# Kernel tuning notes

Measured on AMD Instinct MI355X. Metric: run time of the kernel, lower is better.

The kernel has to match this reference:

```python
import jax, jax.numpy as jnp
import numpy as np

B, C_IN, C_MID, C_OUT, L = 32, 8, 128, 128, 512
T, DT = 50, 0.5
K = T // 2 + 1  # 26
DN = ('NCH', 'OIH', 'NCH')

def conv1d_same(x, w, b):
    # zero-padded 'SAME' Conv1d, kernel size 3
    y = jax.lax.conv_general_dilated(x, w, (1,), 'SAME', dimension_numbers=DN)
    return y + b[None, :, None]

def setup_inputs() -> dict:
    key = jax.random.key(0)
    ks = jax.random.split(key, 32)
    def n(k, shape, s=0.1):
        return jax.random.normal(k, shape, dtype=jnp.float32) * s
    inp = {}
    inp['x'] = jax.random.normal(ks[0], (B, C_IN, L), dtype=jnp.float32)
    # omega encoder (3 convs + ReLU)
    inp['ow1'] = n(ks[1], (C_MID, C_IN, 3));  inp['ob1'] = jnp.zeros((C_MID,), jnp.float32)
    inp['ow2'] = n(ks[2], (C_MID, C_MID, 3)); inp['ob2'] = jnp.zeros((C_MID,), jnp.float32)
    inp['ow3'] = n(ks[3], (C_OUT, C_MID, 3)); inp['ob3'] = jnp.zeros((C_OUT,), jnp.float32)
    # alpha encoder
    inp['aw1'] = n(ks[4], (C_MID, C_IN, 3));  inp['ab1'] = jnp.zeros((C_MID,), jnp.float32)
    inp['aw2'] = n(ks[5], (C_MID, C_MID, 3)); inp['ab2'] = jnp.zeros((C_MID,), jnp.float32)
    inp['aw3'] = n(ks[6], (C_OUT, C_MID, 3)); inp['ab3'] = jnp.zeros((C_OUT,), jnp.float32)
    # hy encoder (4 convs, last Tanh)
    inp['hw1'] = n(ks[7], (C_MID, C_IN, 3));  inp['hb1'] = jnp.zeros((C_MID,), jnp.float32)
    inp['hw2'] = n(ks[8], (C_MID, C_MID, 3)); inp['hb2'] = jnp.zeros((C_MID,), jnp.float32)
    inp['hw3'] = n(ks[9], (C_MID, C_MID, 3)); inp['hb3'] = jnp.zeros((C_MID,), jnp.float32)
    inp['hw4'] = n(ks[10], (C_OUT, C_MID, 3)); inp['hb4'] = jnp.zeros((C_OUT,), jnp.float32)
    # cell circular conv weight (no bias)
    inp['wy'] = n(ks[11], (C_OUT, C_OUT, 3))
    # linear readout
    inp['fct'] = n(ks[12], (K, T))                     # fc_time: T -> K, no bias
    inp['rw1'] = n(ks[13], (64, K * C_OUT)); inp['rb1'] = jnp.zeros((64,), jnp.float32)
    inp['rw2'] = n(ks[14], (32, 64));        inp['rb2'] = jnp.zeros((32,), jnp.float32)
    inp['rw3'] = n(ks[15], (1, 32));         inp['rb3'] = jnp.zeros((1,), jnp.float32)
    return inp

def reference(x, ow1, ob1, ow2, ob2, ow3, ob3,
              aw1, ab1, aw2, ab2, aw3, ab3,
              hw1, hb1, hw2, hb2, hw3, hb3, hw4, hb4,
              wy, fct, rw1, rb1, rw2, rb2, rw3, rb3):
    relu = jax.nn.relu
    omega = relu(conv1d_same(relu(conv1d_same(relu(conv1d_same(x, ow1, ob1)), ow2, ob2)), ow3, ob3))
    alpha = relu(conv1d_same(relu(conv1d_same(relu(conv1d_same(x, aw1, ab1)), aw2, ab2)), aw3, ab3))
    h = relu(conv1d_same(x, hw1, hb1))
    h = relu(conv1d_same(h, hw2, hb2))
    h = relu(conv1d_same(h, hw3, hb3))
    hy0 = jnp.tanh(conv1d_same(h, hw4, hb4))          # (B, C_OUT, L)
    hz0 = jnp.zeros_like(hy0)

    def circ_conv(h):
        # circular padding of 1 on each side, then VALID conv (matches padding_mode='circular')
        hp = jnp.concatenate([h[..., -1:], h, h[..., :1]], axis=-1)
        return jax.lax.conv_general_dilated(hp, wy, (1,), 'VALID', dimension_numbers=DN)

    def step(carry, _):
        hy, hz = carry
        spring = jnp.tanh(circ_conv(hy))
        hz = hz + DT * (spring - omega * hy - alpha * hz)
        hy = hy + DT * hz
        return (hy, hz), hy

    (_, _), ys = jax.lax.scan(step, (hy0, hz0), None, length=T)
    y_seq = jnp.transpose(ys, (1, 0, 2, 3))           # (B, T, C_OUT, L)

    # linear readout: fc_time over T, mean over L, MLP
    fft = jnp.einsum('btcl,kt->bkcl', y_seq, fct)     # (B, K, C_OUT, L)
    feat = fft.reshape(B, K * C_OUT, L).mean(axis=2)  # (B, K*C_OUT)
    h1 = relu(feat @ rw1.T + rb1)
    h2 = relu(h1 @ rw2.T + rb2)
    logits = h2 @ rw3.T + rb3                         # (B, 1)
    return logits, y_seq
```

## Files before the change

kernel.cpp:

```cpp
#include <hip/hip_runtime.h>
#include <math.h>

#define YB (50*128*512)
#define YT (128*512)
#define DTc 0.5f

typedef __attribute__((ext_vector_type(8))) short bf16x8;
typedef __attribute__((ext_vector_type(4))) float f32x4;

__device__ __forceinline__ unsigned short f2bf(float f) {
    unsigned int u = __builtin_bit_cast(unsigned int, f);
    u += 0x7fffu + ((u >> 16) & 1u);
    return (unsigned short)(u >> 16);
}
__device__ __forceinline__ float bf2f(unsigned short h) {
    unsigned int u = ((unsigned int)h) << 16;
    return __builtin_bit_cast(float, u);
}

__device__ __forceinline__ float tanh_fast(float x) {
    float ax = fabsf(x);
    float e  = __expf(-2.f * ax);
    float r  = (1.f - e) * __builtin_amdgcn_rcpf(1.f + e);
    return __builtin_copysignf(r, x);
}

__device__ __forceinline__ void lds_sync() {
    asm volatile("s_waitcnt lgkmcnt(0)" ::: "memory");
    __builtin_amdgcn_sched_barrier(0);
    __builtin_amdgcn_s_barrier();
    __builtin_amdgcn_sched_barrier(0);
}

struct WSrc { const float* p[11]; };
__global__ void wprep_all_k(WSrc s, float* __restrict__ wt) {
    int idx = blockIdx.x * 256 + threadIdx.x;
    if (idx < 9216) {
        int wsel = idx / 3072, r = idx % 3072;
        int row = r >> 7, co = r & 127;
        int ci = row / 3, k = row - ci * 3;
        wt[idx] = s.p[wsel][(co * 8 + ci) * 3 + k];
    } else if (idx < 9216 + 589824) {
        int q = idx - 9216;
        int cv = q / 49152, r = q % 49152;
        int co = r / 384, kap = r % 384;
        int k = kap >> 7;
        int ci = ((kap >> 5) & 3) * 32 + (kap & 31);
        const int selmap[12] = {10, 7, 8, 9, 3, 3, 4, 4, 5, 5, 6, 6};
        float w = s.p[selmap[cv]][(co * 128 + ci) * 3 + k];
        unsigned short hv = f2bf(w);
        unsigned short ov = ((cv >= 4) && (cv & 1)) ? f2bf(w - bf2f(hv)) : hv;
        ((unsigned short*)(wt + 9216))[q] = ov;
    }
}

struct Job { const float* src; float* dst; const float* wt; const float* bias; int sbs, dbs, act; };
struct Jobs3 { Job j[3]; };

__global__ __launch_bounds__(256) void conv8x3_k(Jobs3 js) {
    int jb = blockIdx.y % 3;
    Job jo = js.j[jb];
    int b = blockIdx.z, tile = blockIdx.x, tid = threadIdx.x;
    int l0 = tile * 64;
    int tl4 = (tid & 15) * 4;
    int co0 = (tid >> 4) * 8;
    __shared__ float xs[8 * 68];
    __shared__ float wsh[24 * 128];
    const float* sb = jo.src + (size_t)b * jo.sbs;
    for (int idx = tid; idx < 8 * 66; idx += 256) {
        int ci = idx / 66, ll = idx - ci * 66;
        int gl = l0 - 1 + ll;
        xs[ci * 68 + ll] = (gl >= 0 && gl < 512) ? sb[ci * 512 + gl] : 0.f;
    }
    for (int idx = tid; idx < 24 * 128; idx += 256) wsh[idx] = jo.wt[idx];
    __syncthreads();
    float acc[8][4] = {};
    #pragma unroll
    for (int ci = 0; ci < 8; ++ci) {
        float x6[6];
        #pragma unroll
        for (int j = 0; j < 6; ++j) x6[j] = xs[ci * 68 + tl4 + j];
        #pragma unroll
        for (int k = 0; k < 3; ++k) {
            float w8[8];
            #pragma unroll
            for (int i = 0; i < 8; ++i) w8[i] = wsh[(ci * 3 + k) * 128 + co0 + i];
            #pragma unroll
            for (int i = 0; i < 8; ++i)
                #pragma unroll
                for (int j = 0; j < 4; ++j)
                    acc[i][j] = fmaf(w8[i], x6[k + j], acc[i][j]);
        }
    }
    #pragma unroll
    for (int i = 0; i < 8; ++i) {
        int co = co0 + i;
        float bv = jo.bias[co];
        float4 o;
        o.x = fmaxf(acc[i][0] + bv, 0.f);
        o.y = fmaxf(acc[i][1] + bv, 0.f);
        o.z = fmaxf(acc[i][2] + bv, 0.f);
        o.w = fmaxf(acc[i][3] + bv, 0.f);
        *(float4*)(jo.dst + (size_t)b * jo.dbs + (size_t)co * 512 + l0 + tl4) = o;
    }
}

__global__ __launch_bounds__(512) void mconv_k(
    const float* __restrict__ src, int sbs,
    float* __restrict__ dst, int dbs,
    const unsigned short* __restrict__ w2,
    const float* __restrict__ bias, int act,
    unsigned short* __restrict__ hyt)
{
    int tile = blockIdx.x, b = blockIdx.y;
    int tid = threadIdx.x, lane = tid & 63, wid = tid >> 6;
    int lr = lane & 15, kg = lane >> 4;
    int co = wid * 16 + lr;
    int l0 = tile * 32;

    __shared__ float stage[128 * 40];
    __shared__ uint4 hyX[34 * 16];

    bf16x8 Bw[12];
    {
        const bf16x8* wp = (const bf16x8*)(w2 + (size_t)co * 384);
        #pragma unroll
        for (int s = 0; s < 12; ++s) Bw[s] = wp[s * 4 + kg];
    }

    const float* sb = src + (size_t)b * sbs;
    for (int i = tid; i < 1280; i += 512) {
        int c = i / 10, p4 = (i - c * 10) * 4;
        int l = l0 - 4 + p4;
        f32x4 v;
        if (l >= 0 && l <= 508) {
            v = *(const f32x4*)(sb + (size_t)c * 512 + l);
        } else {
            #pragma unroll
            for (int e = 0; e < 4; ++e) {
                int le = l + e;
                v[e] = (le >= 0 && le < 512) ? sb[(size_t)c * 512 + le] : 0.f;
            }
        }
        *(f32x4*)(stage + c * 40 + p4) = v;
    }
    __syncthreads();
    for (int i = tid; i < 34 * 16; i += 512) {
        int h = i >> 4, c8 = i & 15;
        unsigned short pk[8];
        #pragma unroll
        for (int q = 0; q < 8; ++q) pk[q] = f2bf(stage[(c8 * 8 + q) * 40 + h + 3]);
        hyX[h * 16 + (c8 ^ (h & 7))] = *(uint4*)pk;
    }
    __syncthreads();

    f32x4 acc[2];
    acc[0] = (f32x4){0.f, 0.f, 0.f, 0.f};
    acc[1] = (f32x4){0.f, 0.f, 0.f, 0.f};
    __builtin_amdgcn_s_setprio(1);
    #pragma unroll
    for (int s = 0; s < 12; ++s) {
        int k = s >> 2;
        int chunk = (s & 3) * 4 + kg;
        bf16x8 Bf = Bw[s];
        #pragma unroll
        for (int lt = 0; lt < 2; ++lt) {
            int arow = 16 * lt + lr + k;
            bf16x8 a = __builtin_bit_cast(bf16x8, hyX[arow * 16 + ((arow & 7) ^ chunk)]);
            acc[lt] = __builtin_amdgcn_mfma_f32_16x16x32_bf16(a, Bf, acc[lt], 0, 0, 0);
        }
    }
    __builtin_amdgcn_s_setprio(0);

    float bv = bias[co];
    float vv[2][4];
    #pragma unroll
    for (int lt = 0; lt < 2; ++lt) {
        #pragma unroll
        for (int j = 0; j < 4; ++j) {
            float t = acc[lt][j] + bv;
            vv[lt][j] = (act == 1) ? fmaxf(t, 0.f) : tanh_fast(t);
        }
        *(f32x4*)(dst + (size_t)b * dbs + (size_t)co * 512 + l0 + 16 * lt + 4 * kg) = *(f32x4*)vv[lt];
    }

    if (hyt) {
        lds_sync();
        unsigned short* t16 = (unsigned short*)hyX;
        #pragma unroll
        for (int lt = 0; lt < 2; ++lt)
            #pragma unroll
            for (int j = 0; j < 4; ++j)
                t16[(16 * lt + 4 * kg + j) * 128 + co] = f2bf(vv[lt][j]);
        lds_sync();
        int row = tid >> 4, c8 = tid & 15;
        ((uint4*)hyt)[((size_t)b * 512 + l0 + row) * 16 + c8] =
            ((uint4*)hyX)[row * 16 + c8];
    }
}

struct MJob { const float* src; float* dst; const unsigned short* whi;
              const unsigned short* wlo; const float* bias; int sbs, dbs; };
struct MJobs2 { MJob j[2]; };

__global__ __launch_bounds__(512) void mconv2_k(MJobs2 js) {
    MJob jo = js.j[blockIdx.z];
    int tile = blockIdx.x, b = blockIdx.y;
    int tid = threadIdx.x, lane = tid & 63, wid = tid >> 6;
    int lr = lane & 15, kg = lane >> 4;
    int co = wid * 16 + lr;
    int l0 = tile * 32;

    __shared__ float stage[128 * 40];
    __shared__ uint4 hiX[34 * 16];
    __shared__ uint4 loX[34 * 16];

    const bf16x8* wph = (const bf16x8*)(jo.whi + (size_t)co * 384);
    const bf16x8* wpl = (const bf16x8*)(jo.wlo + (size_t)co * 384);
    bf16x8 Bh[12];
    #pragma unroll
    for (int s = 0; s < 12; ++s) Bh[s] = wph[s * 4 + kg];

    const float* sb = jo.src + (size_t)b * jo.sbs;
    for (int i = tid; i < 1280; i += 512) {
        int c = i / 10, p4 = (i - c * 10) * 4;
        int l = l0 - 4 + p4;
        f32x4 v;
        if (l >= 0 && l <= 508) {
            v = *(const f32x4*)(sb + (size_t)c * 512 + l);
        } else {
            #pragma unroll
            for (int e = 0; e < 4; ++e) {
                int le = l + e;
                v[e] = (le >= 0 && le < 512) ? sb[(size_t)c * 512 + le] : 0.f;
            }
        }
        *(f32x4*)(stage + c * 40 + p4) = v;
    }
    __syncthreads();
    for (int i = tid; i < 34 * 16; i += 512) {
        int h = i >> 4, c8 = i & 15;
        unsigned short ph[8], pl[8];
        #pragma unroll
        for (int q = 0; q < 8; ++q) {
            float x = stage[(c8 * 8 + q) * 40 + h + 3];
            unsigned short hv = f2bf(x);
            ph[q] = hv;
            pl[q] = f2bf(x - bf2f(hv));
        }
        int sx = h * 16 + (c8 ^ (h & 7));
        hiX[sx] = *(uint4*)ph;
        loX[sx] = *(uint4*)pl;
    }
    __syncthreads();

    f32x4 acc[2];
    acc[0] = (f32x4){0.f, 0.f, 0.f, 0.f};
    acc[1] = (f32x4){0.f, 0.f, 0.f, 0.f};
    bf16x8 blc = wpl[kg];
    __builtin_amdgcn_s_setprio(1);
    #pragma unroll
    for (int s = 0; s < 12; ++s) {
        bf16x8 Bl = blc;
        if (s < 11) blc = wpl[(s + 1) * 4 + kg];
        int k = s >> 2;
        int chunk = (s & 3) * 4 + kg;
        #pragma unroll
        for (int lt = 0; lt < 2; ++lt) {
            int arow = 16 * lt + lr + k;
            int ai = arow * 16 + ((arow & 7) ^ chunk);
            bf16x8 ah = __builtin_bit_cast(bf16x8, hiX[ai]);
            bf16x8 al = __builtin_bit_cast(bf16x8, loX[ai]);
            acc[lt] = __builtin_amdgcn_mfma_f32_16x16x32_bf16(ah, Bh[s], acc[lt], 0, 0, 0);
            acc[lt] = __builtin_amdgcn_mfma_f32_16x16x32_bf16(al, Bh[s], acc[lt], 0, 0, 0);
            acc[lt] = __builtin_amdgcn_mfma_f32_16x16x32_bf16(ah, Bl,    acc[lt], 0, 0, 0);
        }
    }
    __builtin_amdgcn_s_setprio(0);

    float bv = jo.bias[co];
    #pragma unroll
    for (int lt = 0; lt < 2; ++lt) {
        float v[4];
        #pragma unroll
        for (int j = 0; j < 4; ++j) v[j] = fmaxf(acc[lt][j] + bv, 0.f);
        *(f32x4*)(jo.dst + (size_t)b * jo.dbs + (size_t)co * 512 + l0 + 16 * lt + 4 * kg) = *(f32x4*)v;
    }
}

__global__ __launch_bounds__(512, 2) void chunk_k(
    const unsigned short* __restrict__ hyt_in,
    unsigned short* __restrict__ hyt_out,
    const float* __restrict__ hy_in,
    const float* __restrict__ hz_in,
    float* __restrict__ hz_out,
    const float* __restrict__ omega, const float* __restrict__ alpha,
    const unsigned short* __restrict__ w2,
    float* __restrict__ ybase,
    float* __restrict__ part, int t0, int ns)
{
    int tile = blockIdx.x, b = blockIdx.y;
    int tid = threadIdx.x, lane = tid & 63, wid = tid >> 6;
    int lr = lane & 15, kg = lane >> 4;
    int co = wid * 16 + lr;
    int l0 = tile * 32;

    __shared__ uint4 hySd[2][800];
    __shared__ float ytmp[2 * 4608];

    bf16x8 Bw[12];
    {
        const bf16x8* wp = (const bf16x8*)(w2 + (size_t)co * 384);
        #pragma unroll
        for (int s = 0; s < 12; ++s) Bw[s] = wp[s * 4 + kg];
    }

    f32x4 hyR[3], hzR[3], omR[3], alR[3];

    {
        const uint4* hsrc = (const uint4*)hyt_in + (size_t)b * 8192;
        for (int i = tid; i < 800; i += 512) {
            int h = i >> 4, c8 = i & 15;
            int l = (l0 - 9 + h) & 511;
            hySd[0][h * 16 + (c8 ^ (h & 7))] = hsrc[l * 16 + c8];
        }
    }
    {
        const float* src = hy_in + (size_t)b * YB;
        size_t ob = (size_t)b * 65536 + (size_t)co * 512;
        #pragma unroll
        for (int lt = 0; lt < 3; ++lt) {
            int l = (l0 - 8 + 16 * lt + 4 * kg) & 511;
            hyR[lt] = *(const f32x4*)(src + (size_t)co * 512 + l);
            omR[lt] = *(const f32x4*)(omega + ob + l);
            alR[lt] = *(const f32x4*)(alpha + ob + l);
            if (t0 > 0) hzR[lt] = *(const f32x4*)(hz_in + ob + l);
            else        hzR[lt] = (f32x4){0.f, 0.f, 0.f, 0.f};
        }
    }
    __syncthreads();

    for (int i = 0; i < ns; ++i) {
        const uint4* hc = &hySd[i & 1][0];
        unsigned short* hn16 = (unsigned short*)&hySd[(i + 1) & 1][0];
        float* yt = ytmp + (i & 1) * 4608;

        f32x4 acc[3];
        #pragma unroll
        for (int lt = 0; lt < 3; ++lt) acc[lt] = (f32x4){0.f, 0.f, 0.f, 0.f};
        __builtin_amdgcn_s_setprio(1);
        #pragma unroll
        for (int s = 0; s < 12; ++s) {
            int chunk = (s & 3) * 4 + kg;
            int k = s >> 2;
            bf16x8 Bf = Bw[s];
            #pragma unroll
            for (int lt = 0; lt < 3; ++lt) {
                int arow = 16 * lt + lr + k;
                bf16x8 a = __builtin_bit_cast(bf16x8, hc[arow * 16 + ((arow & 7) ^ chunk)]);
                acc[lt] = __builtin_amdgcn_mfma_f32_16x16x32_bf16(a, Bf, acc[lt], 0, 0, 0);
            }
        }
        __builtin_amdgcn_s_setprio(0);

        float lsum = 0.f;
        #pragma unroll
        for (int lt = 0; lt < 3; ++lt) {
            #pragma unroll
            for (int j = 0; j < 4; ++j) {
                float spring = tanh_fast(acc[lt][j]);
                float zn = hzR[lt][j] + DTc * (spring - omR[lt][j] * hyR[lt][j] - alR[lt][j] * hzR[lt][j]);
                float hn = hyR[lt][j] + DTc * zn;
                hzR[lt][j] = zn;
                hyR[lt][j] = hn;
            }
            bool valid = (lt == 0) ? (kg >= 2) : (lt == 2) ? (kg < 2) : true;
            int r0 = 16 * lt + 4 * kg;
            if (valid) {
                *(f32x4*)(yt + co * 36 + (r0 - 8)) = hyR[lt];
                lsum += hyR[lt][0] + hyR[lt][1] + hyR[lt][2] + hyR[lt][3];
                if (i == ns - 1)
                    *(f32x4*)(hz_out + (size_t)b * 65536 + (size_t)co * 512 + l0 + (r0 - 8)) = hzR[lt];
            }
            #pragma unroll
            for (int j = 0; j < 4; ++j) {
                int rr = r0 + j + 1;
                int sidx = rr * 128 + (((co >> 3) ^ (rr & 7)) << 3) + (co & 7);
                hn16[sidx] = f2bf(hyR[lt][j]);
            }
        }
        lsum += __shfl_xor(lsum, 16);
        lsum += __shfl_xor(lsum, 32);
        if (kg == 0) part[(((size_t)b * 50 + t0 + i) * 128 + co) * 16 + tile] = lsum;

        lds_sync();

        {
            float* yrow = ybase + (size_t)b * YB + (size_t)i * YT;
            int cs = wid * 16 + (lane >> 3);
            int lq = (lane & 7) * 4;
            #pragma unroll
            for (int cq = 0; cq < 2; ++cq) {
                int c2 = cs + cq * 8;
                f32x4 v = *(const f32x4*)(yt + c2 * 36 + lq);
                *(f32x4*)(yrow + (size_t)c2 * 512 + l0 + lq) = v;
            }
        }
    }

    {
        const uint4* hl = &hySd[ns & 1][0];
        int row = tid >> 4, c8 = tid & 15;
        int h = row + 9;
        ((uint4*)hyt_out)[((size_t)b * 512 + l0 + row) * 16 + c8] =
            hl[h * 16 + (c8 ^ (h & 7))];
    }
}

__global__ __launch_bounds__(256) void readout_k(
    const float* __restrict__ part, const float* __restrict__ fct,
    const float* __restrict__ rw1, const float* __restrict__ rb1,
    const float* __restrict__ rw2, const float* __restrict__ rb2,
    const float* __restrict__ rw3, const float* __restrict__ rb3,
    float* __restrict__ out)
{
    int b = blockIdx.x, tid = threadIdx.x;
    __shared__ float ybar[50 * 128];
    __shared__ float feat[26 * 128];
    __shared__ float h1[64];
    __shared__ float h2[32];
    for (int idx = tid; idx < 50 * 128; idx += 256) {
        const float* p = part + ((size_t)b * 6400 + idx) * 16;
        float s = 0.f;
        #pragma unroll
        for (int q = 0; q < 16; ++q) s += p[q];
        ybar[idx] = s * (1.f / 512.f);
    }
    __syncthreads();
    for (int idx = tid; idx < 26 * 128; idx += 256) {
        int k = idx >> 7, c = idx & 127;
        float s = 0.f;
        for (int t = 0; t < 50; ++t) s += fct[k * 50 + t] * ybar[t * 128 + c];
        feat[idx] = s;
    }
    __syncthreads();
    {
        int j = tid >> 2, q = tid & 3;
        float s = 0.f;
        const float* r = rw1 + (size_t)j * 3328 + q * 832;
        const float* f = feat + q * 832;
        for (int i = 0; i < 832; ++i) s += f[i] * r[i];
        s += __shfl_xor(s, 1);
        s += __shfl_xor(s, 2);
        if (q == 0) h1[j] = fmaxf(s + rb1[j], 0.f);
    }
    __syncthreads();
    if (tid < 32) {
        float s = 0.f;
        for (int i = 0; i < 64; ++i) s += h1[i] * rw2[tid * 64 + i];
        h2[tid] = fmaxf(s + rb2[tid], 0.f);
    }
    __syncthreads();
    if (tid == 0) {
        float s = 0.f;
        for (int i = 0; i < 32; ++i) s += h2[i] * rw3[i];
        out[b] = s + rb3[0];
    }
}

extern "C" void kernel_launch(void* const* d_in, const int* in_sizes, int n_in,
                              void* d_out, int out_size, void* d_ws, size_t ws_size,
                              hipStream_t stream)
{
    const float* x   = (const float*)d_in[0];
    const float* ow1 = (const float*)d_in[1];  const float* ob1 = (const float*)d_in[2];
    const float* ow2 = (const float*)d_in[3];  const float* ob2 = (const float*)d_in[4];
    const float* ow3 = (const float*)d_in[5];  const float* ob3 = (const float*)d_in[6];
    const float* aw1 = (const float*)d_in[7];  const float* ab1 = (const float*)d_in[8];
    const float* aw2 = (const float*)d_in[9];  const float* ab2 = (const float*)d_in[10];
    const float* aw3 = (const float*)d_in[11]; const float* ab3 = (const float*)d_in[12];
    const float* hw1 = (const float*)d_in[13]; const float* hb1 = (const float*)d_in[14];
    const float* hw2 = (const float*)d_in[15]; const float* hb2 = (const float*)d_in[16];
    const float* hw3 = (const float*)d_in[17]; const float* hb3 = (const float*)d_in[18];
    const float* hw4 = (const float*)d_in[19]; const float* hb4 = (const float*)d_in[20];
    const float* wy  = (const float*)d_in[21];
    const float* fct = (const float*)d_in[22];
    const float* rw1 = (const float*)d_in[23]; const float* rb1 = (const float*)d_in[24];
    const float* rw2 = (const float*)d_in[25]; const float* rb2 = (const float*)d_in[26];
    const float* rw3 = (const float*)d_in[27]; const float* rb3 = (const float*)d_in[28];

    float* out  = (float*)d_out;
    float* yout = out + 32;
    float* ws   = (float*)d_ws;

    float* OMEGA = ws;
    float* ALPHA = ws + 2097152;
    float* WT    = ws + 4194304;
    float* PART  = ws + 4498432;
    float* HZ0   = ws + 7775232;
    float* HZ1   = ws + 9872384;
    unsigned short* HYT0 = (unsigned short*)(ws + 11969536);
    unsigned short* HYT1 = (unsigned short*)(ws + 13018112);

    float* To1 = yout + 44 * YT;
    float* Ta1 = yout + 45 * YT;
    float* Th1 = yout + 46 * YT;
    float* To2 = yout + 47 * YT;
    float* Ta2 = yout + 43 * YT;
    float* Th2 = yout + 49 * YT;
    float* Th3 = yout + 42 * YT;
    float* HY0 = yout + 48 * YT;

    float* OW1T = WT + 0;  float* AW1T = WT + 3072;  float* HW1T = WT + 6144;
    unsigned short* U16 = (unsigned short*)(WT + 9216);
    unsigned short* W2WY = U16;
    unsigned short* W2H2 = U16 + 49152;
    unsigned short* W2H3 = U16 + 98304;
    unsigned short* W2H4 = U16 + 147456;
    unsigned short* OW2H = U16 + 196608;  unsigned short* OW2L = U16 + 245760;
    unsigned short* OW3H = U16 + 294912;  unsigned short* OW3L = U16 + 344064;
    unsigned short* AW2H = U16 + 393216;  unsigned short* AW2L = U16 + 442368;
    unsigned short* AW3H = U16 + 491520;  unsigned short* AW3L = U16 + 540672;

    WSrc wsrc;
    wsrc.p[0] = ow1; wsrc.p[1] = aw1; wsrc.p[2] = hw1;
    wsrc.p[3] = ow2; wsrc.p[4] = ow3; wsrc.p[5] = aw2; wsrc.p[6] = aw3;
    wsrc.p[7] = hw2; wsrc.p[8] = hw3; wsrc.p[9] = hw4; wsrc.p[10] = wy;
    wprep_all_k<<<2340, 256, 0, stream>>>(wsrc, WT);

    Jobs3 d1 = {{ {x, To1, OW1T, ob1, 4096, YB, 1},
                  {x, Ta1, AW1T, ab1, 4096, YB, 1},
                  {x, Th1, HW1T, hb1, 4096, YB, 1} }};
    conv8x3_k<<<dim3(8, 3, 32), 256, 0, stream>>>(d1);

    MJobs2 e2 = {{ {To1, To2, OW2H, OW2L, ob2, YB, YB},
                   {Ta1, Ta2, AW2H, AW2L, ab2, YB, YB} }};
    mconv2_k<<<dim3(16, 32, 2), 512, 0, stream>>>(e2);
    MJobs2 e3 = {{ {To2, OMEGA, OW3H, OW3L, ob3, YB, 65536},
                   {Ta2, ALPHA, AW3H, AW3L, ab3, YB, 65536} }};
    mconv2_k<<<dim3(16, 32, 2), 512, 0, stream>>>(e3);

    mconv_k<<<dim3(16, 32), 512, 0, stream>>>(Th1, YB, Th2, YB, W2H2, hb2, 1, nullptr);
    mconv_k<<<dim3(16, 32), 512, 0, stream>>>(Th2, YB, Th3, YB, W2H3, hb3, 1, nullptr);
    mconv_k<<<dim3(16, 32), 512, 0, stream>>>(Th3, YB, HY0, YB, W2H4, hb4, 2, HYT0);

    {
        int t0 = 0, c = 0;
        while (t0 < 50) {
            int ns = (50 - t0 >= 8) ? 8 : (50 - t0);
            const unsigned short* hin = (c & 1) ? HYT1 : HYT0;
            unsigned short* hout      = (c & 1) ? HYT0 : HYT1;
            const float* hyin = (t0 == 0) ? HY0 : (yout + (size_t)(t0 - 1) * YT);
            const float* hzin = (c & 1) ? HZ1 : HZ0;
            float* hzout      = (c & 1) ? HZ0 : HZ1;
            chunk_k<<<dim3(16, 32), 512, 0, stream>>>(hin, hout, hyin, hzin, hzout,
                                                      OMEGA, ALPHA, W2WY,
                                                      yout + (size_t)t0 * YT, PART, t0, ns);
            t0 += ns; ++c;
        }
    }

    readout_k<<<32, 256, 0, stream>>>(PART, fct, rw1, rb1, rw2, rb2, rw3, rb3, out);
}
```

Baseline: 546.2 us.

## Merge encoder conv launches and derive middle-tap MFMA operand via DPP shifts

Combines the omega/alpha dual-precision convs with the hy encoder's single-precision conv into one launch per layer, cutting two kernel launches and giving each launch a larger grid. Inside the recurrent chunk kernel, the middle tap's A operand (row offset +1) is now built from the offset-0 and offset-2 loads with DPP lane shifts instead of a separate LDS read, reducing LDS traffic in the serial timestep loop. This adds VALU permute work and relies on the DPP row-shift pattern matching the 16-lane MFMA row layout.

```diff
diff --git a/kernel.cpp b/kernel.cpp
--- a/kernel.cpp
+++ b/kernel.cpp
@@ -30,6 +30,20 @@
     __builtin_amdgcn_sched_barrier(0);
     __builtin_amdgcn_s_barrier();
     __builtin_amdgcn_sched_barrier(0);
+}
+
+__device__ __forceinline__ uint4 dpp_k1(uint4 a0, uint4 a2) {
+    uint4 r;
+    int t;
+    t = __builtin_amdgcn_update_dpp(0, (int)a0.x, 0x101, 0xF, 0xF, false);
+    r.x = (unsigned)__builtin_amdgcn_update_dpp(t, (int)a2.x, 0x111, 0xF, 0xF, false);
+    t = __builtin_amdgcn_update_dpp(0, (int)a0.y, 0x101, 0xF, 0xF, false);
+    r.y = (unsigned)__builtin_amdgcn_update_dpp(t, (int)a2.y, 0x111, 0xF, 0xF, false);
+    t = __builtin_amdgcn_update_dpp(0, (int)a0.z, 0x101, 0xF, 0xF, false);
+    r.z = (unsigned)__builtin_amdgcn_update_dpp(t, (int)a2.z, 0x111, 0xF, 0xF, false);
+    t = __builtin_amdgcn_update_dpp(0, (int)a0.w, 0x101, 0xF, 0xF, false);
+    r.w = (unsigned)__builtin_amdgcn_update_dpp(t, (int)a2.w, 0x111, 0xF, 0xF, false);
+    return r;
 }
 
 struct WSrc { const float* p[11]; };
@@ -105,11 +119,115 @@
     }
 }
 
+struct UJob { const float* src; float* dst; const unsigned short* whi;
+              const unsigned short* wlo; const float* bias; int sbs, dbs; };
+struct UJobs3 { UJob j[3]; };
+
+__global__ __launch_bounds__(512) void uconv_k(UJobs3 js) {
+    UJob jo = js.j[blockIdx.z];
+    int tile = blockIdx.x, b = blockIdx.y;
+    int tid = threadIdx.x, lane = tid & 63, wid = tid >> 6;
+    int lr = lane & 15, kg = lane >> 4;
+    int co = wid * 16 + lr;
+    int l0 = tile * 32;
+    bool dual = (jo.wlo != nullptr);
+
+    __shared__ float stage[128 * 40];
+    __shared__ uint4 hiX[34 * 16];
+    __shared__ uint4 loX[34 * 16];
+
+    const bf16x8* wph = (const bf16x8*)(jo.whi + (size_t)co * 384);
+    bf16x8 Bh[12];
+    #pragma unroll
+    for (int s = 0; s < 12; ++s) Bh[s] = wph[s * 4 + kg];
+
+    const float* sb = jo.src + (size_t)b * jo.sbs;
+    for (int i = tid; i < 1280; i += 512) {
+        int c = i / 10, p4 = (i - c * 10) * 4;
+        int l = l0 - 4 + p4;
+        f32x4 v;
+        if (l >= 0 && l <= 508) {
+            v = *(const f32x4*)(sb + (size_t)c * 512 + l);
+        } else {
+            #pragma unroll
+            for (int e = 0; e < 4; ++e) {
+                int le = l + e;
+                v[e] = (le >= 0 && le < 512) ? sb[(size_t)c * 512 + le] : 0.f;
+            }
+        }
+        *(f32x4*)(stage + c * 40 + p4) = v;
+    }
+    __syncthreads();
+    for (int i = tid; i < 34 * 16; i += 512) {
+        int h = i >> 4, c8 = i & 15;
+        unsigned short ph[8], pl[8];
+        #pragma unroll
+        for (int q = 0; q < 8; ++q) {
+            float x = stage[(c8 * 8 + q) * 40 + h + 3];
+            unsigned short hv = f2bf(x);
+            ph[q] = hv;
+            pl[q] = f2bf(x - bf2f(hv));
+        }
+        int sx = h * 16 + (c8 ^ (h & 7));
+        hiX[sx] = *(uint4*)ph;
+        if (dual) loX[sx] = *(uint4*)pl;
+    }
+    __syncthreads();
+
+    f32x4 acc[2];
+    acc[0] = (f32x4){0.f, 0.f, 0.f, 0.f};
+    acc[1] = (f32x4){0.f, 0.f, 0.f, 0.f};
+    __builtin_amdgcn_s_setprio(1);
+    if (dual) {
+        const bf16x8* wpl = (const bf16x8*)(jo.wlo + (size_t)co * 384);
+        bf16x8 blc = wpl[kg];
+        #pragma unroll
+        for (int s = 0; s < 12; ++s) {
+            bf16x8 Bl = blc;
+            if (s < 11) blc = wpl[(s + 1) * 4 + kg];
+            int k = s >> 2;
+            int chunk = (s & 3) * 4 + kg;
+            #pragma unroll
+            for (int lt = 0; lt < 2; ++lt) {
+                int arow = 16 * lt + lr + k;
+                int ai = arow * 16 + ((arow & 7) ^ chunk);
+                bf16x8 ah = __builtin_bit_cast(bf16x8, hiX[ai]);
+                bf16x8 al = __builtin_bit_cast(bf16x8, loX[ai]);
+                acc[lt] = __builtin_amdgcn_mfma_f32_16x16x32_bf16(ah, Bh[s], acc[lt], 0, 0, 0);
+                acc[lt] = __builtin_amdgcn_mfma_f32_16x16x32_bf16(al, Bh[s], acc[lt], 0, 0, 0);
+                acc[lt] = __builtin_amdgcn_mfma_f32_16x16x32_bf16(ah, Bl,    acc[lt], 0, 0, 0);
+            }
+        }
+    } else {
+        #pragma unroll
+        for (int s = 0; s < 12; ++s) {
+            int k = s >> 2;
+            int chunk = (s & 3) * 4 + kg;
+            #pragma unroll
+            for (int lt = 0; lt < 2; ++lt) {
+                int arow = 16 * lt + lr + k;
+                bf16x8 ah = __builtin_bit_cast(bf16x8, hiX[arow * 16 + ((arow & 7) ^ chunk)]);
+                acc[lt] = __builtin_amdgcn_mfma_f32_16x16x32_bf16(ah, Bh[s], acc[lt], 0, 0, 0);
+            }
+        }
+    }
+    __builtin_amdgcn_s_setprio(0);
+
+    float bv = jo.bias[co];
+    #pragma unroll
+    for (int lt = 0; lt < 2; ++lt) {
+        float v[4];
+        #pragma unroll
+        for (int j = 0; j < 4; ++j) v[j] = fmaxf(acc[lt][j] + bv, 0.f);
+        *(f32x4*)(jo.dst + (size_t)b * jo.dbs + (size_t)co * 512 + l0 + 16 * lt + 4 * kg) = *(f32x4*)v;
+    }
+}
+
 __global__ __launch_bounds__(512) void mconv_k(
     const float* __restrict__ src, int sbs,
     float* __restrict__ dst, int dbs,
     const unsigned short* __restrict__ w2,
-    const float* __restrict__ bias, int act,
+    const float* __restrict__ bias,
     unsigned short* __restrict__ hyt)
 {
     int tile = blockIdx.x, b = blockIdx.y;
@@ -177,15 +295,13 @@
     #pragma unroll
     for (int lt = 0; lt < 2; ++lt) {
         #pragma unroll
-        for (int j = 0; j < 4; ++j) {
-            float t = acc[lt][j] + bv;
-            vv[lt][j] = (act == 1) ? fmaxf(t, 0.f) : tanh_fast(t);
-        }
+        for (int j = 0; j < 4; ++j)
+            vv[lt][j] = tanh_fast(acc[lt][j] + bv);
         *(f32x4*)(dst + (size_t)b * dbs + (size_t)co * 512 + l0 + 16 * lt + 4 * kg) = *(f32x4*)vv[lt];
     }
 
-    if (hyt) {
-        lds_sync();
+    lds_sync();
+    {
         unsigned short* t16 = (unsigned short*)hyX;
         #pragma unroll
         for (int lt = 0; lt < 2; ++lt)
@@ -196,95 +312,6 @@
         int row = tid >> 4, c8 = tid & 15;
         ((uint4*)hyt)[((size_t)b * 512 + l0 + row) * 16 + c8] =
             ((uint4*)hyX)[row * 16 + c8];
-    }
-}
-
-struct MJob { const float* src; float* dst; const unsigned short* whi;
-              const unsigned short* wlo; const float* bias; int sbs, dbs; };
-struct MJobs2 { MJob j[2]; };
-
-__global__ __launch_bounds__(512) void mconv2_k(MJobs2 js) {
-    MJob jo = js.j[blockIdx.z];
-    int tile = blockIdx.x, b = blockIdx.y;
-    int tid = threadIdx.x, lane = tid & 63, wid = tid >> 6;
-    int lr = lane & 15, kg = lane >> 4;
-    int co = wid * 16 + lr;
-    int l0 = tile * 32;
-
-    __shared__ float stage[128 * 40];
-    __shared__ uint4 hiX[34 * 16];
-    __shared__ uint4 loX[34 * 16];
-
-    const bf16x8* wph = (const bf16x8*)(jo.whi + (size_t)co * 384);
-    const bf16x8* wpl = (const bf16x8*)(jo.wlo + (size_t)co * 384);
-    bf16x8 Bh[12];
-    #pragma unroll
-    for (int s = 0; s < 12; ++s) Bh[s] = wph[s * 4 + kg];
-
-    const float* sb = jo.src + (size_t)b * jo.sbs;
-    for (int i = tid; i < 1280; i += 512) {
-        int c = i / 10, p4 = (i - c * 10) * 4;
-        int l = l0 - 4 + p4;
-        f32x4 v;
-        if (l >= 0 && l <= 508) {
-            v = *(const f32x4*)(sb + (size_t)c * 512 + l);
-        } else {
-            #pragma unroll
-            for (int e = 0; e < 4; ++e) {
-                int le = l + e;
-                v[e] = (le >= 0 && le < 512) ? sb[(size_t)c * 512 + le] : 0.f;
-            }
-        }
-        *(f32x4*)(stage + c * 40 + p4) = v;
-    }
-    __syncthreads();
-    for (int i = tid; i < 34 * 16; i += 512) {
-        int h = i >> 4, c8 = i & 15;
-        unsigned short ph[8], pl[8];
-        #pragma unroll
-        for (int q = 0; q < 8; ++q) {
-            float x = stage[(c8 * 8 + q) * 40 + h + 3];
-            unsigned short hv = f2bf(x);
-            ph[q] = hv;
-            pl[q] = f2bf(x - bf2f(hv));
-        }
-        int sx = h * 16 + (c8 ^ (h & 7));
-        hiX[sx] = *(uint4*)ph;
-        loX[sx] = *(uint4*)pl;
-    }
-    __syncthreads();
-
-    f32x4 acc[2];
-    acc[0] = (f32x4){0.f, 0.f, 0.f, 0.f};
-    acc[1] = (f32x4){0.f, 0.f, 0.f, 0.f};
-    bf16x8 blc = wpl[kg];
-    __builtin_amdgcn_s_setprio(1);
-    #pragma unroll
-    for (int s = 0; s < 12; ++s) {
-        bf16x8 Bl = blc;
-        if (s < 11) blc = wpl[(s + 1) * 4 + kg];
-        int k = s >> 2;
-        int chunk = (s & 3) * 4 + kg;
-        #pragma unroll
-        for (int lt = 0; lt < 2; ++lt) {
-            int arow = 16 * lt + lr + k;
-            int ai = arow * 16 + ((arow & 7) ^ chunk);
-            bf16x8 ah = __builtin_bit_cast(bf16x8, hiX[ai]);
-            bf16x8 al = __builtin_bit_cast(bf16x8, loX[ai]);
-            acc[lt] = __builtin_amdgcn_mfma_f32_16x16x32_bf16(ah, Bh[s], acc[lt], 0, 0, 0);
-            acc[lt] = __builtin_amdgcn_mfma_f32_16x16x32_bf16(al, Bh[s], acc[lt], 0, 0, 0);
-            acc[lt] = __builtin_amdgcn_mfma_f32_16x16x32_bf16(ah, Bl,    acc[lt], 0, 0, 0);
-        }
-    }
-    __builtin_amdgcn_s_setprio(0);
-
-    float bv = jo.bias[co];
-    #pragma unroll
-    for (int lt = 0; lt < 2; ++lt) {
-        float v[4];
-        #pragma unroll
-        for (int j = 0; j < 4; ++j) v[j] = fmaxf(acc[lt][j] + bv, 0.f);
-        *(f32x4*)(jo.dst + (size_t)b * jo.dbs + (size_t)co * 512 + l0 + 16 * lt + 4 * kg) = *(f32x4*)v;
     }
 }
 
@@ -350,15 +377,22 @@
         for (int lt = 0; lt < 3; ++lt) acc[lt] = (f32x4){0.f, 0.f, 0.f, 0.f};
         __builtin_amdgcn_s_setprio(1);
         #pragma unroll
-        for (int s = 0; s < 12; ++s) {
-            int chunk = (s & 3) * 4 + kg;
-            int k = s >> 2;
-            bf16x8 Bf = Bw[s];
+        for (int cs = 0; cs < 4; ++cs) {
+            int chunk = cs * 4 + kg;
+            bf16x8 B0 = Bw[cs], B1 = Bw[cs + 4], B2 = Bw[cs + 8];
             #pragma unroll
             for (int lt = 0; lt < 3; ++lt) {
-                int arow = 16 * lt + lr + k;
-                bf16x8 a = __builtin_bit_cast(bf16x8, hc[arow * 16 + ((arow & 7) ^ chunk)]);
-                acc[lt] = __builtin_amdgcn_mfma_f32_16x16x32_bf16(a, Bf, acc[lt], 0, 0, 0);
+                int r0 = 16 * lt + lr;
+                int r2 = r0 + 2;
+                uint4 a0 = hc[r0 * 16 + ((r0 & 7) ^ chunk)];
+                uint4 a2 = hc[r2 * 16 + ((r2 & 7) ^ chunk)];
+                acc[lt] = __builtin_amdgcn_mfma_f32_16x16x32_bf16(
+                    __builtin_bit_cast(bf16x8, a0), B0, acc[lt], 0, 0, 0);
+                acc[lt] = __builtin_amdgcn_mfma_f32_16x16x32_bf16(
+                    __builtin_bit_cast(bf16x8, a2), B2, acc[lt], 0, 0, 0);
+                uint4 a1 = dpp_k1(a0, a2);
+                acc[lt] = __builtin_amdgcn_mfma_f32_16x16x32_bf16(
+                    __builtin_bit_cast(bf16x8, a1), B1, acc[lt], 0, 0, 0);
             }
         }
         __builtin_amdgcn_s_setprio(0);
@@ -397,11 +431,11 @@
 
         {
             float* yrow = ybase + (size_t)b * YB + (size_t)i * YT;
-            int cs = wid * 16 + (lane >> 3);
+            int cs2 = wid * 16 + (lane >> 3);
             int lq = (lane & 7) * 4;
             #pragma unroll
             for (int cq = 0; cq < 2; ++cq) {
-                int c2 = cs + cq * 8;
+                int c2 = cs2 + cq * 8;
                 f32x4 v = *(const f32x4*)(yt + c2 * 36 + lq);
                 *(f32x4*)(yrow + (size_t)c2 * 512 + l0 + lq) = v;
             }
@@ -533,16 +567,17 @@
                   {x, Th1, HW1T, hb1, 4096, YB, 1} }};
     conv8x3_k<<<dim3(8, 3, 32), 256, 0, stream>>>(d1);
 
-    MJobs2 e2 = {{ {To1, To2, OW2H, OW2L, ob2, YB, YB},
-                   {Ta1, Ta2, AW2H, AW2L, ab2, YB, YB} }};
-    mconv2_k<<<dim3(16, 32, 2), 512, 0, stream>>>(e2);
-    MJobs2 e3 = {{ {To2, OMEGA, OW3H, OW3L, ob3, YB, 65536},
-                   {Ta2, ALPHA, AW3H, AW3L, ab3, YB, 65536} }};
-    mconv2_k<<<dim3(16, 32, 2), 512, 0, stream>>>(e3);
-
-    mconv_k<<<dim3(16, 32), 512, 0, stream>>>(Th1, YB, Th2, YB, W2H2, hb2, 1, nullptr);
-    mconv_k<<<dim3(16, 32), 512, 0, stream>>>(Th2, YB, Th3, YB, W2H3, hb3, 1, nullptr);
-    mconv_k<<<dim3(16, 32), 512, 0, stream>>>(Th3, YB, HY0, YB, W2H4, hb4, 2, HYT0);
+    UJobs3 u2 = {{ {To1, To2, OW2H, OW2L, ob2, YB, YB},
+                   {Ta1, Ta2, AW2H, AW2L, ab2, YB, YB},
+                   {Th1, Th2, W2H2, nullptr, hb2, YB, YB} }};
+    uconv_k<<<dim3(16, 32, 3), 512, 0, stream>>>(u2);
+
+    UJobs3 u3 = {{ {To2, OMEGA, OW3H, OW3L, ob3, YB, 65536},
+                   {Ta2, ALPHA, AW3H, AW3L, ab3, YB, 65536},
+                   {Th2, Th3, W2H3, nullptr, hb3, YB, YB} }};
+    uconv_k<<<dim3(16, 32, 3), 512, 0, stream>>>(u3);
+
+    mconv_k<<<dim3(16, 32), 512, 0, stream>>>(Th3, YB, HY0, YB, W2H4, hb4, HYT0);
 
     {
         int t0 = 0, c = 0;
```

Measured after the change: 537.2 us. No clear change (-1.6%).
